# Optimization experiments

Hardware: AMD Instinct MI355X
Metric: run time of the kernel (lower is better)

## Reference

```python
import jax, jax.numpy as jnp
import numpy as np

N_LEVELS = 16
N_FEATS = 2
LOG2_T = 19
TABLE_SIZE = 2 ** LOG2_T
BASE_RES = 16
FINEST_RES = 2048
N_POINTS = 2_000_000

# growth factor b = (N_max/N_min)^(1/(L-1))
_B = np.exp((np.log(FINEST_RES) - np.log(BASE_RES)) / (N_LEVELS - 1))
# primes[1:4] from the torch module (pi_1 is multiplied into x, etc.)
_PRIMES = np.array([2654435761, 805459861, 3674653429], dtype=np.uint32)
# corner offsets in the same (dx, dy, dz) nesting order as the torch loops
_OFFSETS = np.array([[dx, dy, dz] for dx in (0, 1) for dy in (0, 1) for dz in (0, 1)], dtype=np.int32)


def setup_inputs() -> dict:
    key = jax.random.key(0)
    k1, k2 = jax.random.split(key)
    positions = jax.random.uniform(k1, (N_POINTS, 3), dtype=jnp.float32)  # in [0,1)
    # nn.init.uniform_(table.weight, -1e-4, 1e-4)
    hash_tables = jax.random.uniform(k2, (N_LEVELS, TABLE_SIZE, N_FEATS),
                                     dtype=jnp.float32, minval=-1e-4, maxval=1e-4)
    return {"positions": positions, "hash_tables": hash_tables}


def reference(positions, hash_tables):
    # positions: [N,3] float; hash_tables: [L,T,F] float
    primes = jnp.asarray(_PRIMES)            # uint32
    offsets = jnp.asarray(_OFFSETS)          # [8,3] int32
    off_is_one = (offsets == 1)[None]        # [1,8,3] bool
    feats = []
    for level in range(N_LEVELS):
        res = min(int(BASE_RES * _B ** level), FINEST_RES)
        scaled = positions * (res - 1)                       # [N,3]
        grid = jnp.floor(scaled).astype(jnp.int32)           # [N,3]
        w = scaled - grid.astype(scaled.dtype)               # [N,3] interp weights
        corners = jnp.clip(grid[:, None, :] + offsets[None], 0, res - 1)  # [N,8,3]
        # spatial hash: (x*p1 ^ y*p2 ^ z*p3) mod 2^19. Torch does this in int64;
        # because the modulus is a power of two (low 19 bits) and coords are
        # non-negative, uint32 wraparound arithmetic gives identical results.
        cu = corners.astype(jnp.uint32)
        h = ((cu[..., 0] * primes[0]) ^ (cu[..., 1] * primes[1]) ^ (cu[..., 2] * primes[2]))
        idx = (h % jnp.uint32(TABLE_SIZE)).astype(jnp.int32)  # [N,8]
        cf = hash_tables[level][idx]                          # [N,8,F] gather
        # trilinear corner weights: prod_d (w_d if off_d==1 else 1-w_d)
        cw = jnp.prod(jnp.where(off_is_one, w[:, None, :], 1.0 - w[:, None, :]), axis=-1)  # [N,8]
        feats.append(jnp.sum(cf * cw[..., None], axis=1))    # [N,F]
    return jnp.concatenate(feats, axis=-1)                   # [N, L*F]
```

## Files before the change

### kernel.cpp

```cpp
#include <hip/hip_runtime.h>
#include <math.h>


#define NLV 16
#define TSZ (1 << 19)
#define TMASK (TSZ - 1)
#define BLK 256
#define MAXDENSE 5
#define ROWF2 17
#define ROWF 34

struct P16 {
    int r[NLV];
    int doff[MAXDENSE + 1];
    int ndense;
};

__device__ __forceinline__ float2 enc_level(
    const float px, const float py, const float pz,
    const int res, const float2* __restrict__ tl)
{
    const unsigned P1 = 2654435761u, P2 = 805459861u, P3 = 3674653429u;
    const float scale = (float)(res - 1);
    const float sx = px * scale, sy = py * scale, sz = pz * scale;
    const float fx = floorf(sx), fy = floorf(sy), fz = floorf(sz);
    const float wx = sx - fx, wy = sy - fy, wz = sz - fz;
    const int gx = (int)fx, gy = (int)fy, gz = (int)fz;
    const int rm = res - 1;
    const int x0 = min(max(gx, 0), rm), x1 = min(max(gx + 1, 0), rm);
    const int y0 = min(max(gy, 0), rm), y1 = min(max(gy + 1, 0), rm);
    const int z0 = min(max(gz, 0), rm), z1 = min(max(gz + 1, 0), rm);
    const unsigned hx0 = (unsigned)x0 * P1, hx1 = (unsigned)x1 * P1;
    const unsigned hy0 = (unsigned)y0 * P2, hy1 = (unsigned)y1 * P2;
    const unsigned hz0 = (unsigned)z0 * P3, hz1 = (unsigned)z1 * P3;

    const float2 c000 = tl[(hx0 ^ hy0 ^ hz0) & TMASK];
    const float2 c001 = tl[(hx0 ^ hy0 ^ hz1) & TMASK];
    const float2 c010 = tl[(hx0 ^ hy1 ^ hz0) & TMASK];
    const float2 c011 = tl[(hx0 ^ hy1 ^ hz1) & TMASK];
    const float2 c100 = tl[(hx1 ^ hy0 ^ hz0) & TMASK];
    const float2 c101 = tl[(hx1 ^ hy0 ^ hz1) & TMASK];
    const float2 c110 = tl[(hx1 ^ hy1 ^ hz0) & TMASK];
    const float2 c111 = tl[(hx1 ^ hy1 ^ hz1) & TMASK];

    const float ux = 1.f - wx, uy = 1.f - wy, uz = 1.f - wz;
    const float a00 = ux * uy, a01 = ux * wy, a10 = wx * uy, a11 = wx * wy;
    const float w000 = a00 * uz, w001 = a00 * wz;
    const float w010 = a01 * uz, w011 = a01 * wz;
    const float w100 = a10 * uz, w101 = a10 * wz;
    const float w110 = a11 * uz, w111 = a11 * wz;

    float acc0 = c000.x * w000;           float acc1 = c000.y * w000;
    acc0 += c001.x * w001;                acc1 += c001.y * w001;
    acc0 += c010.x * w010;                acc1 += c010.y * w010;
    acc0 += c011.x * w011;                acc1 += c011.y * w011;
    acc0 += c100.x * w100;                acc1 += c100.y * w100;
    acc0 += c101.x * w101;                acc1 += c101.y * w101;
    acc0 += c110.x * w110;                acc1 += c110.y * w110;
    acc0 += c111.x * w111;                acc1 += c111.y * w111;
    return make_float2(acc0, acc1);
}

__device__ __forceinline__ float2 enc_dense(
    const float px, const float py, const float pz,
    const int res, const float4* __restrict__ G)
{
    const float scale = (float)(res - 1);
    const float sx = px * scale, sy = py * scale, sz = pz * scale;
    int gx = (int)floorf(sx), gy = (int)floorf(sy), gz = (int)floorf(sz);
    gx = min(max(gx, 0), res - 2);
    gy = min(max(gy, 0), res - 2);
    gz = min(max(gz, 0), res - 2);
    const float wx = sx - (float)gx, wy = sy - (float)gy, wz = sz - (float)gz;

    const int r00 = (gz * res + gy) * res + gx;
    const int r10 = r00 + res;
    const int r01 = r00 + res * res;
    const int r11 = r01 + res;
    const float4 v00 = G[r00];
    const float4 v10 = G[r10];
    const float4 v01 = G[r01];
    const float4 v11 = G[r11];

    const float ux = 1.f - wx, uy = 1.f - wy, uz = 1.f - wz;
    const float b00 = uy * uz, b10 = wy * uz, b01 = uy * wz, b11 = wy * wz;
    float acc0 = (v00.x * ux + v00.z * wx) * b00;
    float acc1 = (v00.y * ux + v00.w * wx) * b00;
    acc0 += (v10.x * ux + v10.z * wx) * b10;
    acc1 += (v10.y * ux + v10.w * wx) * b10;
    acc0 += (v01.x * ux + v01.z * wx) * b01;
    acc1 += (v01.y * ux + v01.w * wx) * b01;
    acc0 += (v11.x * ux + v11.z * wx) * b11;
    acc1 += (v11.y * ux + v11.w * wx) * b11;
    return make_float2(acc0, acc1);
}

__global__ __launch_bounds__(BLK) void build_dense_kernel(
    const float* __restrict__ tab, float4* __restrict__ dg,
    const P16 pp, const int total)
{
    const unsigned P1 = 2654435761u, P2 = 805459861u, P3 = 3674653429u;
    const int i = blockIdx.x * BLK + threadIdx.x;
    if (i >= total) return;
    int l = 0;
    #pragma unroll
    for (int k = 1; k < MAXDENSE; ++k)
        if (k < pp.ndense && i >= pp.doff[k]) l = k;
    const int res = pp.r[l], rm = res - 1;
    const int id = i - pp.doff[l];
    const int x = id % res;
    const int t2 = id / res;
    const int y = t2 % res;
    const int z = t2 / res;
    const float2* T = ((const float2*)tab) + (long long)l * TSZ;
    const unsigned hyz = ((unsigned)y * P2) ^ ((unsigned)z * P3);
    const float2 lo = T[(((unsigned)x * P1) ^ hyz) & TMASK];
    const int x1 = min(x + 1, rm);
    const float2 hi = T[(((unsigned)x1 * P1) ^ hyz) & TMASK];
    dg[i] = make_float4(lo.x, lo.y, hi.x, hi.y);
}

__global__ __launch_bounds__(BLK) void pass1_kernel(
    const float* __restrict__ pos,
    const float* __restrict__ tab,
    float2* __restrict__ ws2,
    const float4* __restrict__ dense,
    const P16 pp, const int npts, const int nblk_per_level)
{
    const int level = blockIdx.x / nblk_per_level;
    const int chunk = blockIdx.x % nblk_per_level;
    const long long n = (long long)chunk * BLK + threadIdx.x;
    if (n >= npts) return;

    const float px = pos[n * 3 + 0];
    const float py = pos[n * 3 + 1];
    const float pz = pos[n * 3 + 2];

    float2 f;
    if (level < pp.ndense) {
        f = enc_dense(px, py, pz, pp.r[level], dense + pp.doff[level]);
    } else {
        const float2* tl = ((const float2*)tab) + (long long)level * TSZ;
        f = enc_level(px, py, pz, pp.r[level], tl);
    }
    ws2[(long long)level * npts + n] = f;
}

__global__ __launch_bounds__(BLK) void pass2_kernel(
    const float2* __restrict__ ws2,
    float2* __restrict__ out2,
    const int npts)
{
    __shared__ float2 l2s[BLK * ROWF2];
    const int t = threadIdx.x;
    const long long p0 = (long long)blockIdx.x * BLK;
    const long long n = p0 + t;

    #pragma unroll
    for (int l = 0; l < NLV; ++l) {
        float2 v = make_float2(0.f, 0.f);
        if (n < npts) v = ws2[(long long)l * npts + n];
        l2s[t * ROWF2 + l] = v;
    }
    __syncthreads();

    const long long lim = (long long)npts * NLV;
    const long long obase = p0 * NLV;
    #pragma unroll
    for (int k = 0; k < NLV; ++k) {
        const int idx = k * BLK + t;
        const long long g = obase + idx;
        if (g < lim) {
            const int pt = idx >> 4;
            const int fq = idx & 15;
            out2[g] = l2s[pt * ROWF2 + fq];
        }
    }
}

__global__ __launch_bounds__(BLK) void fused_kernel(
    const float* __restrict__ pos,
    const float* __restrict__ tab,
    float* __restrict__ out,
    const P16 pp, const int npts)
{
    __shared__ float lds[BLK * ROWF];
    const int t = threadIdx.x;
    const long long blk = blockIdx.x;
    const long long n = blk * BLK + t;

    float px = 0.f, py = 0.f, pz = 0.f;
    if (n < npts) {
        px = pos[n * 3 + 0];
        py = pos[n * 3 + 1];
        pz = pos[n * 3 + 2];
    }
    for (int l = 0; l < NLV; ++l) {
        const float2* tl = ((const float2*)tab) + (long long)l * TSZ;
        const float2 f = enc_level(px, py, pz, pp.r[l], tl);
        lds[t * ROWF + 2 * l + 0] = f.x;
        lds[t * ROWF + 2 * l + 1] = f.y;
    }
    __syncthreads();
    float2* o2 = (float2*)out;
    const float2* l2 = (const float2*)lds;
    const long long obase = blk * (BLK * 16);
    const long long lim = (long long)npts * 16;
    #pragma unroll
    for (int k = 0; k < 16; ++k) {
        const long long g = obase + (long long)k * BLK + t;
        if (g < lim) {
            const int lp = (int)((g >> 4) - blk * BLK);
            const int fp = (int)(g & 15);
            o2[g] = l2[lp * 17 + fp];
        }
    }
}

extern "C" void kernel_launch(void* const* d_in, const int* in_sizes, int n_in,
                              void* d_out, int out_size, void* d_ws, size_t ws_size,
                              hipStream_t stream) {
    const float* pos = (const float*)d_in[0];
    const float* tab = (const float*)d_in[1];
    float* out = (float*)d_out;
    const int npts = in_sizes[0] / 3;
    if (npts <= 0) return;

    P16 pp;
    const double B = exp((log(2048.0) - log(16.0)) / 15.0);
    for (int l = 0; l < NLV; ++l) {
        const double v = 16.0 * pow(B, (double)l);
        int r = (int)v;
        if (r > 2048) r = 2048;
        pp.r[l] = r;
    }

    const size_t ws_needed = (size_t)NLV * npts * sizeof(float2);
    const int nblk = (npts + BLK - 1) / BLK;

    pp.ndense = 0;
    long long cum = 0;
    for (int l = 0; l < MAXDENSE; ++l) {
        const long long cells = (long long)pp.r[l] * pp.r[l] * pp.r[l];
        if (ws_needed + (size_t)(cum + cells) * sizeof(float4) <= ws_size) {
            pp.doff[l] = (int)cum;
            cum += cells;
            pp.ndense++;
        } else break;
    }
    for (int l = pp.ndense; l <= MAXDENSE; ++l) pp.doff[l] = (int)cum;

    if (ws_size >= ws_needed) {
        float2* ws2 = (float2*)d_ws;
        float4* dense = (float4*)((char*)d_ws + ws_needed);
        if (pp.ndense > 0) {
            const int total = (int)cum;
            hipLaunchKernelGGL(build_dense_kernel, dim3((total + BLK - 1) / BLK), dim3(BLK),
                               0, stream, tab, dense, pp, total);
        }
        hipLaunchKernelGGL(pass1_kernel, dim3(nblk * NLV), dim3(BLK), 0, stream,
                           pos, tab, ws2, dense, pp, npts, nblk);
        hipLaunchKernelGGL(pass2_kernel, dim3(nblk), dim3(BLK), 0, stream,
                           ws2, (float2*)out, npts);
    } else {
        hipLaunchKernelGGL(fused_kernel, dim3(nblk), dim3(BLK), 0, stream,
                           pos, tab, out, pp, npts);
    }
}
```

Before: 1.291 ms.

## Store intermediate per-level features as half2 and allow more dense levels

```diff
diff --git a/kernel.cpp b/kernel.cpp
--- a/kernel.cpp
+++ b/kernel.cpp
@@ -1,4 +1,5 @@
 #include <hip/hip_runtime.h>
+#include <hip/hip_fp16.h>
 #include <math.h>
 
 
@@ -6,8 +7,8 @@
 #define TSZ (1 << 19)
 #define TMASK (TSZ - 1)
 #define BLK 256
-#define MAXDENSE 5
-#define ROWF2 17
+#define MAXDENSE 7
+#define ROWH2 (NLV + 1)
 #define ROWF 34
 
 struct P16 {
@@ -82,7 +83,8 @@
     const float4 v01 = G[r01];
     const float4 v11 = G[r11];
 
-    const float ux = 1.f - wx, uy = 1.f - wy, uz = 1.f - wz;
+    const float ux = 1.f - wx;
+    const float uy = 1.f - wy, uz = 1.f - wz;
     const float b00 = uy * uz, b10 = wy * uz, b01 = uy * wz, b11 = wy * wz;
     float acc0 = (v00.x * ux + v00.z * wx) * b00;
     float acc1 = (v00.y * ux + v00.w * wx) * b00;
@@ -123,7 +125,7 @@
 __global__ __launch_bounds__(BLK) void pass1_kernel(
     const float* __restrict__ pos,
     const float* __restrict__ tab,
-    float2* __restrict__ ws2,
+    __half2* __restrict__ wsh,
     const float4* __restrict__ dense,
     const P16 pp, const int npts, const int nblk_per_level)
 {
@@ -143,37 +145,47 @@
         const float2* tl = ((const float2*)tab) + (long long)level * TSZ;
         f = enc_level(px, py, pz, pp.r[level], tl);
     }
-    ws2[(long long)level * npts + n] = f;
+    wsh[(long long)level * npts + n] = __float22half2_rn(f);
 }
 
 __global__ __launch_bounds__(BLK) void pass2_kernel(
-    const float2* __restrict__ ws2,
-    float2* __restrict__ out2,
+    const __half2* __restrict__ wsh,
+    float4* __restrict__ out4,
     const int npts)
 {
-    __shared__ float2 l2s[BLK * ROWF2];
+    __shared__ __half2 l2s[BLK][ROWH2];
     const int t = threadIdx.x;
     const long long p0 = (long long)blockIdx.x * BLK;
-    const long long n = p0 + t;
-
-    #pragma unroll
-    for (int l = 0; l < NLV; ++l) {
-        float2 v = make_float2(0.f, 0.f);
-        if (n < npts) v = ws2[(long long)l * npts + n];
-        l2s[t * ROWF2 + l] = v;
+
+    #pragma unroll
+    for (int k = 0; k < 8; ++k) {
+        const int idx = k * BLK + t;
+        const int l = idx >> 7;
+        const int j = idx & 127;
+        const long long base = p0 + 2 * j;
+        union { uint2 u; __half2 h[2]; } cv;
+        cv.u = make_uint2(0u, 0u);
+        const __half2* src = wsh + (long long)l * npts + p0;
+        if (base + 1 < npts) {
+            cv.u = ((const uint2*)src)[j];
+        } else if (base < npts) {
+            cv.h[0] = src[2 * j];
+        }
+        l2s[2 * j + 0][l] = cv.h[0];
+        l2s[2 * j + 1][l] = cv.h[1];
     }
     __syncthreads();
 
-    const long long lim = (long long)npts * NLV;
-    const long long obase = p0 * NLV;
-    #pragma unroll
-    for (int k = 0; k < NLV; ++k) {
+    #pragma unroll
+    for (int k = 0; k < 8; ++k) {
         const int idx = k * BLK + t;
-        const long long g = obase + idx;
-        if (g < lim) {
-            const int pt = idx >> 4;
-            const int fq = idx & 15;
-            out2[g] = l2s[pt * ROWF2 + fq];
+        const int pt = idx >> 3;
+        const int q = idx & 7;
+        const long long np = p0 + pt;
+        if (np < npts) {
+            const float2 a = __half22float2(l2s[pt][2 * q + 0]);
+            const float2 b = __half22float2(l2s[pt][2 * q + 1]);
+            out4[np * 8 + q] = make_float4(a.x, a.y, b.x, b.y);
         }
     }
 }
@@ -235,7 +247,7 @@
         pp.r[l] = r;
     }
 
-    const size_t ws_needed = (size_t)NLV * npts * sizeof(float2);
+    const size_t ws_needed = (size_t)NLV * npts * sizeof(__half2);
     const int nblk = (npts + BLK - 1) / BLK;
 
     pp.ndense = 0;
@@ -251,7 +263,7 @@
     for (int l = pp.ndense; l <= MAXDENSE; ++l) pp.doff[l] = (int)cum;
 
     if (ws_size >= ws_needed) {
-        float2* ws2 = (float2*)d_ws;
+        __half2* wsh = (__half2*)d_ws;
         float4* dense = (float4*)((char*)d_ws + ws_needed);
         if (pp.ndense > 0) {
             const int total = (int)cum;
@@ -259,9 +271,9 @@
                                0, stream, tab, dense, pp, total);
         }
         hipLaunchKernelGGL(pass1_kernel, dim3(nblk * NLV), dim3(BLK), 0, stream,
-                           pos, tab, ws2, dense, pp, npts, nblk);
+                           pos, tab, wsh, dense, pp, npts, nblk);
         hipLaunchKernelGGL(pass2_kernel, dim3(nblk), dim3(BLK), 0, stream,
-                           ws2, (float2*)out, npts);
+                           wsh, (float4*)out, npts);
     } else {
         hipLaunchKernelGGL(fused_kernel, dim3(nblk), dim3(BLK), 0, stream,
                            pos, tab, out, pp, npts);
```

Result: no change. 1.305 ms (+1.0%).
